# Kernel optimization log

Hardware: AMD Instinct MI355X
Metric: run time of the kernel (lower is better)

## Reference

```python
import jax, jax.numpy as jnp
import numpy as np

HEADS = 4
DIM_QK = 128
DIM_V = 128
FMAP = 32  # H = W = 32, L = 1024
DIM = 512
B = 16


def rel_to_abs(x):
    # x: [B, Nh, L, 2L-1] -> [B, Nh, L, L]
    b, nh, L, _ = x.shape
    x = jnp.pad(x, ((0, 0), (0, 0), (0, 0), (0, 1)))          # [B, Nh, L, 2L]
    flat = x.reshape(b, nh, L * 2 * L)
    flat = jnp.pad(flat, ((0, 0), (0, 0), (0, L - 1)))
    final = flat.reshape(b, nh, L + 1, 2 * L - 1)
    return final[:, :, :L, L - 1:]


def relative_logits_1d(q, rel_k):
    # q: [B, Nh, H, W, d], rel_k: [2W-1, d] -> [B, Nh, H, H, W, W]
    b, nh, h, w, _ = q.shape
    rl = jnp.einsum('bnhwd,md->bnhwm', q, rel_k)
    rl = rl.reshape(b, nh * h, w, 2 * w - 1)
    rl = rel_to_abs(rl)                                        # [B, Nh*H, W, W]
    rl = rl.reshape(b, nh, h, w, w)
    rl = jnp.broadcast_to(rl[:, :, :, None], (b, nh, h, h, w, w))
    return rl


def rel_pos_logits(q, rel_height, rel_width):
    # q: [B, Nh, L, d] with L = FMAP*FMAP -> [B, Nh, L, L]
    b, nh, L, d = q.shape
    h = w = FMAP
    q5 = q.reshape(b, nh, h, w, d)
    # width logits: 'b n x i y j -> b n (x y) (i j)'
    rw = relative_logits_1d(q5, rel_width)
    rw = rw.transpose(0, 1, 2, 4, 3, 5).reshape(b, nh, h * w, h * w)
    # height logits: transpose spatial, then 'b n x i y j -> b n (y x) (j i)'
    rh = relative_logits_1d(q5.transpose(0, 1, 3, 2, 4), rel_height)
    rh = rh.transpose(0, 1, 4, 2, 5, 3).reshape(b, nh, h * w, h * w)
    return rw + rh


def setup_inputs() -> dict:
    key = jax.random.key(0)
    k1, k2, k3, k4, k5 = jax.random.split(key, 5)
    scale = DIM_QK ** -0.5
    return {
        'featuremap': jax.random.normal(k1, (B, DIM, FMAP, FMAP), jnp.float32),
        'w_qk': jax.random.normal(k2, (2 * HEADS * DIM_QK, DIM), jnp.float32) * (DIM ** -0.5),
        'w_v': jax.random.normal(k3, (HEADS * DIM_V, DIM), jnp.float32) * (DIM ** -0.5),
        'rel_height': jax.random.normal(k4, (2 * FMAP - 1, DIM_QK), jnp.float32) * scale,
        'rel_width': jax.random.normal(k5, (2 * FMAP - 1, DIM_QK), jnp.float32) * scale,
    }


def reference(featuremap, w_qk, w_v, rel_height, rel_width):
    b, c, h, w = featuremap.shape
    L = h * w
    # 1x1 convs (no bias) == channel matmuls
    qk = jnp.einsum('bchw,oc->bohw', featuremap, w_qk)
    q, k = jnp.split(qk, 2, axis=1)
    v = jnp.einsum('bchw,oc->bohw', featuremap, w_v)

    def to_heads(x, d):
        # 'B (h d) H W -> B h (H W) d'
        return x.reshape(b, HEADS, d, L).transpose(0, 1, 3, 2)

    q = to_heads(q, DIM_QK) * (DIM_QK ** -0.5)
    k = to_heads(k, DIM_QK)
    v = to_heads(v, DIM_V)

    logits = jnp.einsum('bhxd,bhyd->bhxy', q, k)
    logits = logits + rel_pos_logits(q, rel_height, rel_width)
    weights = jax.nn.softmax(logits, axis=-1)
    attn = jnp.einsum('bhxy,bhyd->bhxd', weights, v)
    # 'B h (H W) d -> B (h d) H W'
    out = attn.transpose(0, 1, 3, 2).reshape(b, HEADS * DIM_V, h, w)
    return out
```

## Files before the change

### kernel.cpp

```cpp
#include <hip/hip_runtime.h>
#include <hip/hip_bf16.h>
#include <math.h>

typedef __bf16 bf16x8 __attribute__((ext_vector_type(8)));
typedef float f32x4 __attribute__((ext_vector_type(4)));

#define QSCALE_L2E (0.08838834764831845f * 1.4426950408889634f)

static __device__ __forceinline__ unsigned short bits_bf16(float v) {
  __hip_bfloat16 h = __float2bfloat16(v);
  return *reinterpret_cast<unsigned short*>(&h);
}

static __device__ __forceinline__ void gload16(const void* g, void* l) {
  __builtin_amdgcn_global_load_lds(
      (const __attribute__((address_space(1))) void*)g,
      (__attribute__((address_space(3))) void*)l, 16, 0, 0);
}

__global__ __launch_bounds__(256) void k_convw(const float* __restrict__ wqk,
                                               const float* __restrict__ wv,
                                               const float* __restrict__ relw,
                                               const float* __restrict__ relh,
                                               __hip_bfloat16* __restrict__ wall,
                                               __hip_bfloat16* __restrict__ relsb) {
  int i = blockIdx.x * 256 + threadIdx.x;
  if (i < 1536 * 512) {
    float v = (i < 1024 * 512) ? wqk[i] : wv[i - 1024 * 512];
    wall[i] = __float2bfloat16(v);
  } else {
    int j = i - 1536 * 512;
    int t = j >> 13, m = (j >> 7) & 63, d = j & 127;
    float v = (m < 63) ? (t ? relh[m * 128 + d] : relw[m * 128 + d]) : 0.f;
    relsb[j] = __float2bfloat16(v);
  }
}

__global__ __launch_bounds__(256) void k_tfm(const float* __restrict__ fm,
                                             __hip_bfloat16* __restrict__ fmt) {
  __shared__ float t[64][65];
  int lt = blockIdx.x, ct = blockIdx.y, b = blockIdx.z;
  int tid = threadIdx.x;
  const float* src = fm + ((size_t)b * 512 + ct * 64) * 1024 + lt * 64;
#pragma unroll
  for (int i = 0; i < 16; ++i) {
    int idx = i * 256 + tid;
    int r = idx >> 6, cl = idx & 63;
    t[r][cl] = src[(size_t)r * 1024 + cl];
  }
  __syncthreads();
  __hip_bfloat16* dst = fmt + ((size_t)b * 1024 + lt * 64) * 512 + ct * 64;
#pragma unroll
  for (int i = 0; i < 16; ++i) {
    int idx = i * 256 + tid;
    int r = idx >> 6, cc = idx & 63;
    dst[(size_t)r * 512 + cc] = __float2bfloat16(t[cc][r]);
  }
}

__global__ __launch_bounds__(256) void k_gemm(const __hip_bfloat16* __restrict__ fmt,
                                              const __hip_bfloat16* __restrict__ wall,
                                              __hip_bfloat16* __restrict__ Qb,
                                              __hip_bfloat16* __restrict__ Kb,
                                              __hip_bfloat16* __restrict__ Vt) {
  __shared__ char smem[32768];
  char* As = smem;
  char* Bs = smem + 16384;
  int bm = blockIdx.x, bn = blockIdx.y, b = blockIdx.z;
  int tid = threadIdx.x;
  int lane = tid & 63, wave = tid >> 6;
  int wr = wave >> 1, wc = wave & 1;
  int g = lane >> 4, ln = lane & 15;
  const char* Ag = (const char*)(fmt + ((size_t)b * 1024 + bm * 128) * 512);
  const char* Bg = (const char*)(wall + (size_t)bn * 128 * 512);

  int j3 = lane >> 3, j7 = lane & 7;
  int segsrc = ((j7 ^ j3) << 4);

  f32x4 acc[4][4] = {};
  for (int kb = 0; kb < 8; ++kb) {
#pragma unroll
    for (int i = 0; i < 4; ++i) {
      int R = (wave * 4 + i) * 8;
      size_t go = (size_t)(R + j3) * 1024 + (size_t)kb * 128 + segsrc;
      gload16(Ag + go, As + R * 128);
      gload16(Bg + go, Bs + R * 128);
    }
    __syncthreads();
#pragma unroll
    for (int ks = 0; ks < 2; ++ks) {
      int kcol = ks * 64 + (g << 4);
      bf16x8 af[4], bfr[4];
#pragma unroll
      for (int m = 0; m < 4; ++m) {
        int row = wr * 64 + m * 16 + ln;
        af[m] = *(const bf16x8*)(As + row * 128 + (kcol ^ ((ln & 7) << 4)));
      }
#pragma unroll
      for (int n = 0; n < 4; ++n) {
        int row = wc * 64 + n * 16 + ln;
        bfr[n] = *(const bf16x8*)(Bs + row * 128 + (kcol ^ ((ln & 7) << 4)));
      }
#pragma unroll
      for (int m = 0; m < 4; ++m)
#pragma unroll
        for (int n = 0; n < 4; ++n)
          acc[m][n] = __builtin_amdgcn_mfma_f32_16x16x32_bf16(af[m], bfr[n], acc[m][n], 0, 0, 0);
    }
    __syncthreads();
  }

  int otype = bn >> 2;
  int head = bn & 3;
  if (otype != 2) {
    float sc = (otype == 0) ? QSCALE_L2E : 1.0f;
#pragma unroll
    for (int m = 0; m < 4; ++m)
#pragma unroll
      for (int n = 0; n < 4; ++n) {
        int d = wc * 64 + n * 16 + ln;
#pragma unroll
        for (int r = 0; r < 4; ++r) {
          int l = wr * 64 + m * 16 + g * 4 + r;
          *(__hip_bfloat16*)(smem + l * 256 + ((d * 2) ^ ((l & 7) << 4))) =
              __float2bfloat16(acc[m][n][r] * sc);
        }
      }
    __syncthreads();
    __hip_bfloat16* dstb =
        (otype == 0 ? Qb : Kb) + (((size_t)(b * 4 + head) * 1024) + bm * 128) * 128;
#pragma unroll
    for (int i = 0; i < 8; ++i) {
      int idx = i * 256 + tid;
      int row = idx >> 4, c16 = idx & 15;
      uint4 v = *(const uint4*)(smem + row * 256 + ((c16 * 16) ^ ((row & 7) << 4)));
      *(uint4*)(dstb + (size_t)row * 128 + c16 * 8) = v;
    }
  } else {
#pragma unroll
    for (int m = 0; m < 4; ++m)
#pragma unroll
      for (int n = 0; n < 4; ++n) {
        int d = wc * 64 + n * 16 + ln;
        int lbase = wr * 64 + m * 16 + g * 4;
        ushort4 pk;
        pk.x = bits_bf16(acc[m][n][0]);
        pk.y = bits_bf16(acc[m][n][1]);
        pk.z = bits_bf16(acc[m][n][2]);
        pk.w = bits_bf16(acc[m][n][3]);
        *(ushort4*)(smem + d * 256 + ((lbase * 2) ^ ((d & 7) << 4))) = pk;
      }
    __syncthreads();
    __hip_bfloat16* dstb = Vt + ((size_t)(b * 4 + head) * 128) * 1024 + bm * 128;
#pragma unroll
    for (int i = 0; i < 8; ++i) {
      int idx = i * 256 + tid;
      int row = idx >> 4, c16 = idx & 15;
      uint4 v = *(const uint4*)(smem + row * 256 + ((c16 * 16) ^ ((row & 7) << 4)));
      *(uint4*)(dstb + (size_t)row * 1024 + c16 * 8) = v;
    }
  }
}

__global__ __launch_bounds__(256) void k_bias(const __hip_bfloat16* __restrict__ Qb,
                                              const __hip_bfloat16* __restrict__ relsb,
                                              float* __restrict__ QRW,
                                              float* __restrict__ QRH) {
  __shared__ char sh[32768];
  int bx = blockIdx.x, bh = blockIdx.y;
  int tid = threadIdx.x, lane = tid & 63, wave = tid >> 6;
  int g = lane >> 4, ln = lane & 15;
#pragma unroll
  for (int i = 0; i < 8; ++i) {
    int chunk = i * 256 + tid;
    int row = chunk >> 4, c16 = chunk & 15;
    *(uint4*)(sh + row * 256 + ((c16 * 16) ^ ((row & 7) << 4))) =
        *(const uint4*)(relsb + (size_t)row * 128 + c16 * 8);
  }
  __syncthreads();
  size_t bhL = (size_t)bh * 1024;
  int l0 = bx * 128 + wave * 32;
  const __hip_bfloat16* Qg = Qb + (bhL + l0) * 128;
  bf16x8 a[2][4];
#pragma unroll
  for (int lf = 0; lf < 2; ++lf)
#pragma unroll
    for (int ks = 0; ks < 4; ++ks)
      a[lf][ks] = *(const bf16x8*)(Qg + (size_t)(lf * 16 + ln) * 128 + ks * 32 + g * 8);
#pragma unroll
  for (int t = 0; t < 2; ++t) {
    float* dst = (t == 0 ? QRW : QRH) + (bhL + l0) * 64;
#pragma unroll
    for (int n = 0; n < 4; ++n) {
      f32x4 acc2[2] = {};
#pragma unroll
      for (int ks = 0; ks < 4; ++ks) {
        int mrow = n * 16 + ln;
        bf16x8 bf = *(const bf16x8*)(sh + t * 16384 + mrow * 256 +
                                     ((ks * 64 + g * 16) ^ ((mrow & 7) << 4)));
#pragma unroll
        for (int lf = 0; lf < 2; ++lf)
          acc2[lf] = __builtin_amdgcn_mfma_f32_16x16x32_bf16(a[lf][ks], bf, acc2[lf], 0, 0, 0);
      }
#pragma unroll
      for (int lf = 0; lf < 2; ++lf)
#pragma unroll
        for (int r = 0; r < 4; ++r)
          dst[(size_t)(lf * 16 + g * 4 + r) * 64 + n * 16 + ln] = acc2[lf][r];
    }
  }
}

__global__ __launch_bounds__(256, 2) void k_attn(const __hip_bfloat16* __restrict__ Qb,
                                                 const __hip_bfloat16* __restrict__ Kb,
                                                 const __hip_bfloat16* __restrict__ Vt,
                                                 const float* __restrict__ QRW,
                                                 const float* __restrict__ QRH,
                                                 float* __restrict__ out) {
  extern __shared__ char smem[];
  float* hb_s = (float*)smem;
  char* kv = smem + 20480;
  char* vtl = smem + 36864;
  char* pt = smem + 53248;

  int qt = blockIdx.x, bh = blockIdx.y;
  int b = bh >> 2, h = bh & 3;
  int tid = threadIdx.x, lane = tid & 63, wave = tid >> 6;
  int g = lane >> 4, ln = lane & 15;
  int q0 = qt * 128;
  size_t bhL = (size_t)bh * 1024;

#pragma unroll
  for (int i = 0; i < 5; ++i) {
    int c = i * 256 + tid;
    if (c < 1152) {
      int row = c / 9, j = c % 9;
      int s0 = (31 - ((q0 + row) >> 5)) & ~3;
      *(uint4*)(hb_s + row * 40 + j * 4) =
          *(const uint4*)(QRH + (bhL + q0 + row) * 64 + s0 + j * 4);
    }
  }

  bf16x8 qa[2][4];
  float wb[2][2][4];
  int qloc[2], hbase[2];
#pragma unroll
  for (int u = 0; u < 2; ++u) {
    qloc[u] = wave * 32 + u * 16 + ln;
    int qg = q0 + qloc[u];
    int cx = qg & 31, rx = qg >> 5;
    hbase[u] = (31 - rx) & 3;
    const __hip_bfloat16* qrow = Qb + (bhL + qg) * 128;
#pragma unroll
    for (int ks = 0; ks < 4; ++ks)
      qa[u][ks] = *(const bf16x8*)(qrow + ks * 32 + g * 8);
    const float* wrow = QRW + (bhL + qg) * 64 + (31 - cx) + g * 4;
#pragma unroll
    for (int half = 0; half < 2; ++half)
#pragma unroll
      for (int r = 0; r < 4; ++r) wb[u][half][r] = wrow[half * 16 + r];
  }

  f32x4 acc[2][8] = {};
  float mrow[2] = {-1e30f, -1e30f}, lrow[2] = {0.f, 0.f};
  char* pw = pt + wave * 4096;
  const char* Kg0 = (const char*)(Kb + bhL * 128);
  const char* Vg0 = (const char*)(Vt + (size_t)bh * 128 * 1024);
  int j3 = lane >> 3, j7 = lane & 7;
  int segv = ((j7 ^ j3) << 4);

  for (int kt = 0; kt < 16; ++kt) {
    __syncthreads();
    const char* Kg = Kg0 + (size_t)kt * 64 * 256;
#pragma unroll
    for (int i = 0; i < 4; ++i) {
      int R = (wave * 4 + i) * 4;
      int seg = ((lane & 15) ^ (((i & 1) * 4) + (lane >> 4))) << 4;
      gload16(Kg + (size_t)(R + (lane >> 4)) * 256 + seg, kv + R * 256);
    }
    const char* Vg = Vg0 + (size_t)kt * 128;
#pragma unroll
    for (int i = 0; i < 4; ++i) {
      int R = (wave * 4 + i) * 8;
      gload16(Vg + (size_t)(R + j3) * 2048 + segv, vtl + R * 128);
    }
    __syncthreads();

    f32x4 s[2][4] = {};
#pragma unroll
    for (int ks = 0; ks < 4; ++ks) {
      int kcol = ks * 64 + (g << 4);
#pragma unroll
      for (int n = 0; n < 4; ++n) {
        int krow = n * 16 + ln;
        bf16x8 kf = *(const bf16x8*)(kv + krow * 256 + (kcol ^ ((krow & 7) << 4)));
        s[0][n] = __builtin_amdgcn_mfma_f32_16x16x32_bf16(kf, qa[0][ks], s[0][n], 0, 0, 0);
        s[1][n] = __builtin_amdgcn_mfma_f32_16x16x32_bf16(kf, qa[1][ks], s[1][n], 0, 0, 0);
      }
    }
#pragma unroll
    for (int u = 0; u < 2; ++u) {
      float hb0 = hb_s[qloc[u] * 40 + hbase[u] + kt * 2];
      float hb1 = hb_s[qloc[u] * 40 + hbase[u] + kt * 2 + 1];
#pragma unroll
      for (int n = 0; n < 4; ++n) {
        float hb = (n >> 1) ? hb1 : hb0;
#pragma unroll
        for (int r = 0; r < 4; ++r) s[u][n][r] += wb[u][n & 1][r] + hb;
      }
      float mt = s[u][0][0];
#pragma unroll
      for (int n = 0; n < 4; ++n)
#pragma unroll
        for (int r = 0; r < 4; ++r) mt = fmaxf(mt, s[u][n][r]);
      mt = fmaxf(mt, __shfl_xor(mt, 16, 64));
      mt = fmaxf(mt, __shfl_xor(mt, 32, 64));
      float mn = fmaxf(mrow[u], mt);
      float alpha = exp2f(mrow[u] - mn);
      mrow[u] = mn;
      float rs = 0.f;
#pragma unroll
      for (int n = 0; n < 4; ++n)
#pragma unroll
        for (int r = 0; r < 4; ++r) {
          s[u][n][r] = exp2f(s[u][n][r] - mn);
          rs += s[u][n][r];
        }
      rs += __shfl_xor(rs, 16, 64);
      rs += __shfl_xor(rs, 32, 64);
      lrow[u] = lrow[u] * alpha + rs;
#pragma unroll
      for (int mf = 0; mf < 8; ++mf) acc[u][mf] *= alpha;
#pragma unroll
      for (int n = 0; n < 4; ++n) {
        ushort4 pk;
        pk.x = bits_bf16(s[u][n][0]);
        pk.y = bits_bf16(s[u][n][1]);
        pk.z = bits_bf16(s[u][n][2]);
        pk.w = bits_bf16(s[u][n][3]);
        *(ushort4*)(pw + (u * 16 + ln) * 128 + ((n * 32 + g * 8) ^ ((ln & 7) << 4))) = pk;
      }
    }
#pragma unroll
    for (int ks2 = 0; ks2 < 2; ++ks2) {
      int kcb = ks2 * 64 + (g << 4);
      bf16x8 pb0 = *(const bf16x8*)(pw + ln * 128 + (kcb ^ ((ln & 7) << 4)));
      bf16x8 pb1 = *(const bf16x8*)(pw + (16 + ln) * 128 + (kcb ^ ((ln & 7) << 4)));
#pragma unroll
      for (int mf = 0; mf < 8; ++mf) {
        int vrow = mf * 16 + ln;
        bf16x8 av = *(const bf16x8*)(vtl + vrow * 128 + (kcb ^ ((vrow & 7) << 4)));
        acc[0][mf] = __builtin_amdgcn_mfma_f32_16x16x32_bf16(av, pb0, acc[0][mf], 0, 0, 0);
        acc[1][mf] = __builtin_amdgcn_mfma_f32_16x16x32_bf16(av, pb1, acc[1][mf], 0, 0, 0);
      }
    }
  }
#pragma unroll
  for (int u = 0; u < 2; ++u) {
    float linv = 1.0f / lrow[u];
    int qg3 = q0 + wave * 32 + u * 16 + ln;
#pragma unroll
    for (int mf = 0; mf < 8; ++mf) {
      int dbase = mf * 16 + g * 4;
#pragma unroll
      for (int r = 0; r < 4; ++r) {
        out[((size_t)(b * 512 + h * 128 + dbase + r)) * 1024 + qg3] = acc[u][mf][r] * linv;
      }
    }
  }
}

extern "C" void kernel_launch(void* const* d_in, const int* in_sizes, int n_in,
                              void* d_out, int out_size, void* d_ws, size_t ws_size,
                              hipStream_t stream) {
  const float* fm = (const float*)d_in[0];
  const float* wqk = (const float*)d_in[1];
  const float* wv = (const float*)d_in[2];
  const float* relh = (const float*)d_in[3];
  const float* relw = (const float*)d_in[4];
  float* out = (float*)d_out;
  char* w = (char*)d_ws;

  __hip_bfloat16* fmt = (__hip_bfloat16*)w;
  __hip_bfloat16* wall = (__hip_bfloat16*)(w + 16777216);
  __hip_bfloat16* Qb = (__hip_bfloat16*)(w + 18350080);
  __hip_bfloat16* Kb = (__hip_bfloat16*)(w + 35127296);
  __hip_bfloat16* Vt = (__hip_bfloat16*)(w + 51904512);
  float* QRW = (float*)(w + 68681728);
  float* QRH = (float*)(w + 85458944);
  __hip_bfloat16* relsb = (__hip_bfloat16*)(w + 102236160);

  k_convw<<<3136, 256, 0, stream>>>(wqk, wv, relw, relh, wall, relsb);
  k_tfm<<<dim3(16, 8, 16), 256, 0, stream>>>(fm, fmt);
  k_gemm<<<dim3(8, 12, 16), 256, 0, stream>>>(fmt, wall, Qb, Kb, Vt);
  k_bias<<<dim3(8, 64), 256, 0, stream>>>(Qb, relsb, QRW, QRH);
  k_attn<<<dim3(8, 64), 256, 69632, stream>>>(Qb, Kb, Vt, QRW, QRH, out);
}
```

Before: 132.1 us.

## Double-buffer K/V tiles in attention with larger 256-query blocks

The attention kernel now uses 512-thread blocks covering 256 queries, so each loaded K/V tile is reused by twice as many waves. K/V tiles are double-buffered in LDS, with the next tile's async global->LDS load issued before computing on the current one, which removes one barrier per iteration. MFMA sections are wrapped with s_setprio. The cost is 136KB of LDS per block, which limits each CU to one block, and a grid of 256 blocks.

```diff
diff --git a/kernel.cpp b/kernel.cpp
--- a/kernel.cpp
+++ b/kernel.cpp
@@ -211,7 +211,7 @@
   }
 }
 
-__global__ __launch_bounds__(256, 2) void k_attn(const __hip_bfloat16* __restrict__ Qb,
+__global__ __launch_bounds__(512, 2) void k_attn(const __hip_bfloat16* __restrict__ Qb,
                                                  const __hip_bfloat16* __restrict__ Kb,
                                                  const __hip_bfloat16* __restrict__ Vt,
                                                  const float* __restrict__ QRW,
@@ -219,21 +219,21 @@
                                                  float* __restrict__ out) {
   extern __shared__ char smem[];
   float* hb_s = (float*)smem;
-  char* kv = smem + 20480;
-  char* vtl = smem + 36864;
-  char* pt = smem + 53248;
-
-  int qt = blockIdx.x, bh = blockIdx.y;
+  char* kbuf = smem + 40960;
+  char* vbuf = smem + 40960 + 32768;
+  char* pt = smem + 40960 + 65536;
+
+  int bh = blockIdx.x, qt = blockIdx.y;
   int b = bh >> 2, h = bh & 3;
   int tid = threadIdx.x, lane = tid & 63, wave = tid >> 6;
   int g = lane >> 4, ln = lane & 15;
-  int q0 = qt * 128;
+  int q0 = qt * 256;
   size_t bhL = (size_t)bh * 1024;
 
 #pragma unroll
   for (int i = 0; i < 5; ++i) {
-    int c = i * 256 + tid;
-    if (c < 1152) {
+    int c = i * 512 + tid;
+    if (c < 2304) {
       int row = c / 9, j = c % 9;
       int s0 = (31 - ((q0 + row) >> 5)) & ~3;
       *(uint4*)(hb_s + row * 40 + j * 4) =
@@ -261,43 +261,56 @@
       for (int r = 0; r < 4; ++r) wb[u][half][r] = wrow[half * 16 + r];
   }
 
-  f32x4 acc[2][8] = {};
-  float mrow[2] = {-1e30f, -1e30f}, lrow[2] = {0.f, 0.f};
-  char* pw = pt + wave * 4096;
   const char* Kg0 = (const char*)(Kb + bhL * 128);
   const char* Vg0 = (const char*)(Vt + (size_t)bh * 128 * 1024);
   int j3 = lane >> 3, j7 = lane & 7;
   int segv = ((j7 ^ j3) << 4);
 
+  auto STAGE = [&](int bsel, int kt2) {
+    const char* Kg = Kg0 + (size_t)kt2 * 64 * 256;
+    char* kvb = kbuf + bsel * 16384;
+#pragma unroll
+    for (int i = 0; i < 2; ++i) {
+      int R = (wave * 2 + i) * 4;
+      int seg = ((lane & 15) ^ ((i & 1) * 4 + (lane >> 4))) << 4;
+      gload16(Kg + (size_t)(R + (lane >> 4)) * 256 + seg, kvb + R * 256);
+    }
+    const char* Vg = Vg0 + (size_t)kt2 * 128;
+    char* vtb = vbuf + bsel * 16384;
+#pragma unroll
+    for (int i = 0; i < 2; ++i) {
+      int R = (wave * 2 + i) * 8;
+      gload16(Vg + (size_t)(R + j3) * 2048 + segv, vtb + R * 128);
+    }
+  };
+
+  f32x4 acc[2][8] = {};
+  float mrow[2] = {-1e30f, -1e30f}, lrow[2] = {0.f, 0.f};
+  char* pw = pt + wave * 4096;
+
+  STAGE(0, 0);
+  __syncthreads();
+
   for (int kt = 0; kt < 16; ++kt) {
-    __syncthreads();
-    const char* Kg = Kg0 + (size_t)kt * 64 * 256;
-#pragma unroll
-    for (int i = 0; i < 4; ++i) {
-      int R = (wave * 4 + i) * 4;
-      int seg = ((lane & 15) ^ (((i & 1) * 4) + (lane >> 4))) << 4;
-      gload16(Kg + (size_t)(R + (lane >> 4)) * 256 + seg, kv + R * 256);
-    }
-    const char* Vg = Vg0 + (size_t)kt * 128;
-#pragma unroll
-    for (int i = 0; i < 4; ++i) {
-      int R = (wave * 4 + i) * 8;
-      gload16(Vg + (size_t)(R + j3) * 2048 + segv, vtl + R * 128);
-    }
-    __syncthreads();
+    int cur = kt & 1;
+    if (kt < 15) STAGE(cur ^ 1, kt + 1);
+    char* kvb = kbuf + cur * 16384;
+    char* vtb = vbuf + cur * 16384;
 
     f32x4 s[2][4] = {};
+    __builtin_amdgcn_s_setprio(1);
 #pragma unroll
     for (int ks = 0; ks < 4; ++ks) {
       int kcol = ks * 64 + (g << 4);
 #pragma unroll
       for (int n = 0; n < 4; ++n) {
         int krow = n * 16 + ln;
-        bf16x8 kf = *(const bf16x8*)(kv + krow * 256 + (kcol ^ ((krow & 7) << 4)));
+        bf16x8 kf = *(const bf16x8*)(kvb + krow * 256 + (kcol ^ ((krow & 7) << 4)));
         s[0][n] = __builtin_amdgcn_mfma_f32_16x16x32_bf16(kf, qa[0][ks], s[0][n], 0, 0, 0);
         s[1][n] = __builtin_amdgcn_mfma_f32_16x16x32_bf16(kf, qa[1][ks], s[1][n], 0, 0, 0);
       }
     }
+    __builtin_amdgcn_s_setprio(0);
 #pragma unroll
     for (int u = 0; u < 2; ++u) {
       float hb0 = hb_s[qloc[u] * 40 + hbase[u] + kt * 2];
@@ -341,6 +354,7 @@
         *(ushort4*)(pw + (u * 16 + ln) * 128 + ((n * 32 + g * 8) ^ ((ln & 7) << 4))) = pk;
       }
     }
+    __builtin_amdgcn_s_setprio(1);
 #pragma unroll
     for (int ks2 = 0; ks2 < 2; ++ks2) {
       int kcb = ks2 * 64 + (g << 4);
@@ -349,11 +363,13 @@
 #pragma unroll
       for (int mf = 0; mf < 8; ++mf) {
         int vrow = mf * 16 + ln;
-        bf16x8 av = *(const bf16x8*)(vtl + vrow * 128 + (kcb ^ ((vrow & 7) << 4)));
+        bf16x8 av = *(const bf16x8*)(vtb + vrow * 128 + (kcb ^ ((vrow & 7) << 4)));
         acc[0][mf] = __builtin_amdgcn_mfma_f32_16x16x32_bf16(av, pb0, acc[0][mf], 0, 0, 0);
         acc[1][mf] = __builtin_amdgcn_mfma_f32_16x16x32_bf16(av, pb1, acc[1][mf], 0, 0, 0);
       }
     }
+    __builtin_amdgcn_s_setprio(0);
+    __syncthreads();
   }
 #pragma unroll
   for (int u = 0; u < 2; ++u) {
@@ -390,9 +406,12 @@
   float* QRH = (float*)(w + 85458944);
   __hip_bfloat16* relsb = (__hip_bfloat16*)(w + 102236160);
 
+  hipFuncSetAttribute((const void*)k_attn,
+                      hipFuncAttributeMaxDynamicSharedMemorySize, 139264);
+
   k_convw<<<3136, 256, 0, stream>>>(wqk, wv, relw, relh, wall, relsb);
   k_tfm<<<dim3(16, 8, 16), 256, 0, stream>>>(fm, fmt);
   k_gemm<<<dim3(8, 12, 16), 256, 0, stream>>>(fmt, wall, Qb, Kb, Vt);
   k_bias<<<dim3(8, 64), 256, 0, stream>>>(Qb, relsb, QRW, QRH);
-  k_attn<<<dim3(8, 64), 256, 69632, stream>>>(Qb, Kb, Vt, QRW, QRH, out);
-}
+  k_attn<<<dim3(64, 4), 512, 139264, stream>>>(Qb, Kb, Vt, QRW, QRH, out);
+}
```

New measurement: 125.4 us, median of 2. 1.05x faster.
